# Kernel optimization log

Measured on AMD Instinct MI355X. Metric: run time of the kernel, lower is better.

Reference implementation:

```python
import jax, jax.numpy as jnp
import numpy as np

# Irreps: in1 = 128x0e + 64x1o + 32x2e, in2 = 16x0e (one-hot-style species attr),
# out = 128x0e + 64x1o + 32x2e.  (mul_in, mul_out, l) per CG path (l x 0e -> l).
PATHS = [(128, 128, 0), (64, 64, 1), (32, 32, 2)]
N_SPECIES = 16
N_NODES = 200_000
DIM_IN = sum(u * (2 * l + 1) for u, _, l in PATHS)   # 480
DIM_OUT = sum(w * (2 * l + 1) for _, w, l in PATHS)  # 480


def setup_inputs() -> dict:
    key = jax.random.key(0)
    k = jax.random.split(key, 5)
    return {
        "x": jax.random.normal(k[0], (N_NODES, DIM_IN), dtype=jnp.float32),
        "operand": jax.random.uniform(k[1], (N_NODES, N_SPECIES), dtype=jnp.float32),
        "w0": jax.random.normal(k[2], (128, N_SPECIES, 128), dtype=jnp.float32),
        "w1": jax.random.normal(k[3], (64, N_SPECIES, 64), dtype=jnp.float32),
        "w2": jax.random.normal(k[4], (32, N_SPECIES, 32), dtype=jnp.float32),
    }


def _path(xl, operand, W, alpha):
    # out[z,w,k] = alpha * sum_{u,v} xl[z,u,k] * operand[z,v] * W[u,v,w]
    # Scan over the small species axis v to avoid a huge [Z,u,w] intermediate.
    Z, u, d = xl.shape
    wm = W.shape[2]

    def step(acc, vin):
        Wv, ov = vin  # Wv: [u, w_out], ov: [Z]
        return acc + ov[:, None, None] * jnp.einsum('zuk,uw->zwk', xl, Wv), None

    init = jnp.zeros((Z, wm, d), dtype=xl.dtype)
    out, _ = jax.lax.scan(step, init, (jnp.moveaxis(W, 1, 0), operand.T))
    return alpha * out


def _fctp(x, operand, weights):
    # e3nn FullyConnectedTensorProduct with in2 = pure 0e scalars:
    # w3j(l, 0, l) = I / sqrt(2l+1); path_weight (component/element norm)
    # = sqrt((2l+1) / (mul_in * n_species))  ->  net alpha = 1/sqrt(mul_in*n_species).
    outs, off = [], 0
    for (u, wm, l), W in zip(PATHS, weights):
        d = 2 * l + 1
        xl = x[:, off:off + u * d].reshape(-1, u, d)  # [Z, mul_in, 2l+1]
        off += u * d
        alpha = jnp.float32(1.0 / float(np.sqrt(u * operand.shape[1])))
        out_l = _path(xl, operand, W, alpha)          # [Z, mul_out, 2l+1]
        outs.append(out_l.reshape(-1, wm * d))
    return jnp.concatenate(outs, axis=-1)             # [Z, 480]


def reference(x, operand, w0, w1, w2):
    return _fctp(x, operand, (w0, w1, w2))
```

## Files before the change

kernel.cpp:

```cpp
#include <hip/hip_runtime.h>
#include <stdint.h>


typedef __attribute__((ext_vector_type(8))) short bf16x8;
typedef __attribute__((ext_vector_type(4))) float f32x4;

__device__ __forceinline__ unsigned short f2bf(float f) {
    unsigned int u = __float_as_uint(f);
    u += 0x7fffu + ((u >> 16) & 1u);
    return (unsigned short)(u >> 16);
}
__device__ __forceinline__ unsigned int pack2(float a, float b) {
    return (unsigned int)f2bf(a) | ((unsigned int)f2bf(b) << 16);
}

__global__ void prep_wt(const float* __restrict__ w0, const float* __restrict__ w1,
                        const float* __restrict__ w2, unsigned short* __restrict__ wt) {
    int i = blockIdx.x * 256 + threadIdx.x;
    if (i < 262144) {
        int kk = i & 2047;
        int w  = i >> 11;
        wt[i] = f2bf(w0[kk * 128 + w]);
    } else if (i < 327680) {
        int r = i - 262144;
        int kk = r & 1023, w = r >> 10;
        wt[i] = f2bf(w1[kk * 64 + w]);
    } else if (i < 344064) {
        int r = i - 327680;
        int kk = r & 511, w = r >> 9;
        wt[i] = f2bf(w2[kk * 32 + w]);
    }
}

template<int D, int OFF, int K, int BN, int BM, int WAVES_M, int WAVES_N>
__global__ __launch_bounds__(256, 2)
void fctp_gemm(const float* __restrict__ x, const float* __restrict__ op,
               const unsigned short* __restrict__ wt, float* __restrict__ out,
               int Z, float alpha)
{
    constexpr int BK   = 32;
    constexpr int LDA  = BK + 8;
    constexpr int NSTEP = K / BK;
    constexpr int WTM  = BM / WAVES_M;
    constexpr int WTN  = BN / WAVES_N;
    constexpr int TM   = WTM / 16;
    constexpr int TN   = WTN / 16;

    __shared__ unsigned short Asm_[BM * LDA];
    __shared__ unsigned short Bsm_[BN * LDA];

    const int tid = threadIdx.x;
    const int M   = Z * D;
    const long m0 = (long)blockIdx.x * BM;

    int arow, usel;
    if constexpr (BM == 128) { arow = tid & 127; usel = tid >> 7; }
    else                     { arow = tid;       usel = 0;        }

    long mr = m0 + arow;
    if (mr >= M) mr = M - 1;
    const int zr = (int)(mr / D);
    const int kr = (int)(mr % D);

    float oreg[16];
    #pragma unroll
    for (int v = 0; v < 16; ++v) oreg[v] = op[(size_t)zr * 16 + v];

    const float* xp = x + (size_t)zr * 480 + OFF + kr + usel * D;

    f32x4 acc[TM][TN];
    #pragma unroll
    for (int i = 0; i < TM; ++i)
        #pragma unroll
        for (int j = 0; j < TN; ++j) acc[i][j] = f32x4{0.f, 0.f, 0.f, 0.f};

    const int lane = tid & 63;
    const int wv   = tid >> 6;
    const int wm0  = (wv / WAVES_N) * WTM;
    const int wn0  = (wv % WAVES_N) * WTN;
    const int q    = lane >> 4;
    const int l16  = lane & 15;

    for (int s = 0; s < NSTEP; ++s) {
        const int k0 = s * BK;
        __syncthreads();

        constexpr int BTOT = BN * 4;
        #pragma unroll
        for (int it = 0; it < (BTOT + 255) / 256; ++it) {
            int idx = it * 256 + tid;
            if ((BTOT % 256 == 0) || (idx < BTOT)) {
                int n = idx >> 2, qq = idx & 3;
                *(uint4*)(&Bsm_[n * LDA + qq * 8]) =
                    *(const uint4*)(wt + (size_t)n * K + k0 + qq * 8);
            }
        }

        if constexpr (BM == 128) {
            float xv = *xp; xp += 2 * D;
            unsigned int pk[8];
            #pragma unroll
            for (int vv = 0; vv < 8; ++vv)
                pk[vv] = pack2(xv * oreg[2 * vv], xv * oreg[2 * vv + 1]);
            uint4* dst = (uint4*)(&Asm_[arow * LDA + usel * 16]);
            dst[0] = uint4{pk[0], pk[1], pk[2], pk[3]};
            dst[1] = uint4{pk[4], pk[5], pk[6], pk[7]};
        } else {
            float xv0 = xp[0], xv1 = xp[D]; xp += 2 * D;
            unsigned int pk[16];
            #pragma unroll
            for (int vv = 0; vv < 8; ++vv) {
                pk[vv]     = pack2(xv0 * oreg[2 * vv], xv0 * oreg[2 * vv + 1]);
                pk[8 + vv] = pack2(xv1 * oreg[2 * vv], xv1 * oreg[2 * vv + 1]);
            }
            uint4* dst = (uint4*)(&Asm_[arow * LDA]);
            dst[0] = uint4{pk[0],  pk[1],  pk[2],  pk[3]};
            dst[1] = uint4{pk[4],  pk[5],  pk[6],  pk[7]};
            dst[2] = uint4{pk[8],  pk[9],  pk[10], pk[11]};
            dst[3] = uint4{pk[12], pk[13], pk[14], pk[15]};
        }
        __syncthreads();

        bf16x8 af[TM], bfr[TN];
        #pragma unroll
        for (int i = 0; i < TM; ++i)
            af[i] = *(const bf16x8*)(&Asm_[(wm0 + i * 16 + l16) * LDA + q * 8]);
        #pragma unroll
        for (int j = 0; j < TN; ++j)
            bfr[j] = *(const bf16x8*)(&Bsm_[(wn0 + j * 16 + l16) * LDA + q * 8]);
        #pragma unroll
        for (int i = 0; i < TM; ++i)
            #pragma unroll
            for (int j = 0; j < TN; ++j)
                acc[i][j] = __builtin_amdgcn_mfma_f32_16x16x32_bf16(
                    af[i], bfr[j], acc[i][j], 0, 0, 0);
    }

    #pragma unroll
    for (int i = 0; i < TM; ++i) {
        #pragma unroll
        for (int p = 0; p < 4; ++p) {
            long m = m0 + wm0 + i * 16 + q * 4 + p;
            if (m < M) {
                int z = (int)(m / D);
                int k = (int)(m % D);
                float* orow = out + (size_t)z * 480 + OFF + k;
                #pragma unroll
                for (int j = 0; j < TN; ++j) {
                    int col = wn0 + j * 16 + l16;
                    orow[col * D] = alpha * acc[i][j][p];
                }
            }
        }
    }
}

extern "C" void kernel_launch(void* const* d_in, const int* in_sizes, int n_in,
                              void* d_out, int out_size, void* d_ws, size_t ws_size,
                              hipStream_t stream) {
    (void)n_in; (void)out_size; (void)ws_size;
    const float* x  = (const float*)d_in[0];
    const float* op = (const float*)d_in[1];
    const float* w0 = (const float*)d_in[2];
    const float* w1 = (const float*)d_in[3];
    const float* w2 = (const float*)d_in[4];
    float* out = (float*)d_out;
    const int Z = in_sizes[0] / 480;

    unsigned short* wt = (unsigned short*)d_ws;
    prep_wt<<<1344, 256, 0, stream>>>(w0, w1, w2, wt);

    const unsigned short* wt0 = wt;
    const unsigned short* wt1 = wt + 262144;
    const unsigned short* wt2 = wt + 327680;

    {
        int M = Z, BM = 128;
        fctp_gemm<1, 0, 2048, 128, 128, 2, 2>
            <<<(M + BM - 1) / BM, 256, 0, stream>>>(x, op, wt0, out, Z, 0.02209708691f);
    }
    {
        int M = Z * 3, BM = 256;
        fctp_gemm<3, 128, 1024, 64, 256, 2, 2>
            <<<(M + BM - 1) / BM, 256, 0, stream>>>(x, op, wt1, out, Z, 0.03125f);
    }
    {
        int M = Z * 5, BM = 256;
        fctp_gemm<5, 320, 512, 32, 256, 4, 1>
            <<<(M + BM - 1) / BM, 256, 0, stream>>>(x, op, wt2, out, Z, 0.04419417382f);
    }
}
```

Baseline: 910.4 us.

## Double-buffer GEMM with async global-to-LDS weight loads, fp16 MFMA, swizzled LDS

Restructures the per-path GEMM main loop to double-buffer the A and B tiles in shared memory. B tiles are fetched with asynchronous global_load_lds DMA from a pre-swizzled weight layout, which removes the padded LDS rows and the register round trip. BK grows from 32 to 64, and the A operand (x times operand outer product) is built with packed fp16 multiplies instead of manual bf16 rounding, feeding f16 MFMA. The aim is to overlap the next tile's loads and A construction with the current MFMAs and to halve the number of barriers. In exchange it adds fp16 range and precision risk and uses more LDS per block.

```diff
diff --git a/kernel.cpp b/kernel.cpp
--- a/kernel.cpp
+++ b/kernel.cpp
@@ -2,34 +2,37 @@
 #include <stdint.h>
 
 
-typedef __attribute__((ext_vector_type(8))) short bf16x8;
+typedef __attribute__((ext_vector_type(8))) _Float16 f16x8;
+typedef __attribute__((ext_vector_type(2))) _Float16 f16x2;
 typedef __attribute__((ext_vector_type(4))) float f32x4;
-
-__device__ __forceinline__ unsigned short f2bf(float f) {
-    unsigned int u = __float_as_uint(f);
-    u += 0x7fffu + ((u >> 16) & 1u);
-    return (unsigned short)(u >> 16);
-}
-__device__ __forceinline__ unsigned int pack2(float a, float b) {
-    return (unsigned int)f2bf(a) | ((unsigned int)f2bf(b) << 16);
-}
 
 __global__ void prep_wt(const float* __restrict__ w0, const float* __restrict__ w1,
                         const float* __restrict__ w2, unsigned short* __restrict__ wt) {
     int i = blockIdx.x * 256 + threadIdx.x;
+    int n, kk, BN, base;
+    float v;
     if (i < 262144) {
-        int kk = i & 2047;
-        int w  = i >> 11;
-        wt[i] = f2bf(w0[kk * 128 + w]);
+        base = 0;      n = i >> 11; kk = i & 2047; BN = 128;
+        v = w0[kk * 128 + n];
     } else if (i < 327680) {
         int r = i - 262144;
-        int kk = r & 1023, w = r >> 10;
-        wt[i] = f2bf(w1[kk * 64 + w]);
-    } else if (i < 344064) {
+        base = 262144; n = r >> 10; kk = r & 1023; BN = 64;
+        v = w1[kk * 64 + n];
+    } else {
         int r = i - 327680;
-        int kk = r & 511, w = r >> 9;
-        wt[i] = f2bf(w2[kk * 32 + w]);
-    }
+        base = 327680; n = r >> 9;  kk = r & 511;  BN = 32;
+        v = w2[kk * 32 + n];
+    }
+    int t = kk >> 6, c = kk & 63;
+    union { _Float16 h; unsigned short s; } u;
+    u.h = (_Float16)v;
+    wt[base + (t * BN + n) * 64 + (c ^ ((n & 7) * 8))] = u.s;
+}
+
+__device__ __forceinline__ void gl_lds16(const void* g, void* l) {
+    __builtin_amdgcn_global_load_lds(
+        (const __attribute__((address_space(1))) unsigned int*)g,
+        (__attribute__((address_space(3))) unsigned int*)l, 16, 0, 0);
 }
 
 template<int D, int OFF, int K, int BN, int BM, int WAVES_M, int WAVES_N>
@@ -38,16 +41,17 @@
                const unsigned short* __restrict__ wt, float* __restrict__ out,
                int Z, float alpha)
 {
-    constexpr int BK   = 32;
-    constexpr int LDA  = BK + 8;
+    constexpr int BK    = 64;
     constexpr int NSTEP = K / BK;
-    constexpr int WTM  = BM / WAVES_M;
-    constexpr int WTN  = BN / WAVES_N;
-    constexpr int TM   = WTM / 16;
-    constexpr int TN   = WTN / 16;
-
-    __shared__ unsigned short Asm_[BM * LDA];
-    __shared__ unsigned short Bsm_[BN * LDA];
+    constexpr int WTM   = BM / WAVES_M;
+    constexpr int WTN   = BN / WAVES_N;
+    constexpr int TM    = WTM / 16;
+    constexpr int TN    = WTN / 16;
+    constexpr int CPW   = BN / 32;
+    constexpr int NXL   = (BM == 128) ? 2 : 4;
+
+    __shared__ unsigned short Asm_[2][BM * 64];
+    __shared__ unsigned short Bsm_[2][BN * 64];
 
     const int tid = threadIdx.x;
     const int M   = Z * D;
@@ -62,17 +66,16 @@
     const int zr = (int)(mr / D);
     const int kr = (int)(mr % D);
 
-    float oreg[16];
+    f16x2 oh[8];
     #pragma unroll
-    for (int v = 0; v < 16; ++v) oreg[v] = op[(size_t)zr * 16 + v];
-
-    const float* xp = x + (size_t)zr * 480 + OFF + kr + usel * D;
-
-    f32x4 acc[TM][TN];
-    #pragma unroll
-    for (int i = 0; i < TM; ++i)
-        #pragma unroll
-        for (int j = 0; j < TN; ++j) acc[i][j] = f32x4{0.f, 0.f, 0.f, 0.f};
+    for (int j = 0; j < 8; ++j) {
+        float a = op[(size_t)zr * 16 + 2 * j];
+        float b = op[(size_t)zr * 16 + 2 * j + 1];
+        oh[j] = f16x2{(_Float16)a, (_Float16)b};
+    }
+
+    const float* xbase = x + (size_t)zr * 480 + OFF + kr;
+    if constexpr (BM == 128) xbase += usel * 2 * D;
 
     const int lane = tid & 63;
     const int wv   = tid >> 6;
@@ -81,59 +84,86 @@
     const int q    = lane >> 4;
     const int l16  = lane & 15;
 
-    for (int s = 0; s < NSTEP; ++s) {
-        const int k0 = s * BK;
-        __syncthreads();
-
-        constexpr int BTOT = BN * 4;
-        #pragma unroll
-        for (int it = 0; it < (BTOT + 255) / 256; ++it) {
-            int idx = it * 256 + tid;
-            if ((BTOT % 256 == 0) || (idx < BTOT)) {
-                int n = idx >> 2, qq = idx & 3;
-                *(uint4*)(&Bsm_[n * LDA + qq * 8]) =
-                    *(const uint4*)(wt + (size_t)n * K + k0 + qq * 8);
-            }
-        }
-
-        if constexpr (BM == 128) {
-            float xv = *xp; xp += 2 * D;
+    f32x4 acc[TM][TN];
+    #pragma unroll
+    for (int i = 0; i < TM; ++i)
+        #pragma unroll
+        for (int j = 0; j < TN; ++j) acc[i][j] = f32x4{0.f, 0.f, 0.f, 0.f};
+
+    float xr[NXL];
+
+    auto xload = [&](int tt) {
+        #pragma unroll
+        for (int u = 0; u < NXL; ++u) xr[u] = xbase[(size_t)tt * 4 * D + u * D];
+    };
+
+    auto buildA = [&](int buf) {
+        unsigned short* rowp = &Asm_[buf][arow * 64];
+        const int swz = (arow & 7) * 8;
+        #pragma unroll
+        for (int u = 0; u < NXL; ++u) {
+            _Float16 xh = (_Float16)xr[u];
+            f16x2 xb2{xh, xh};
             unsigned int pk[8];
             #pragma unroll
-            for (int vv = 0; vv < 8; ++vv)
-                pk[vv] = pack2(xv * oreg[2 * vv], xv * oreg[2 * vv + 1]);
-            uint4* dst = (uint4*)(&Asm_[arow * LDA + usel * 16]);
-            dst[0] = uint4{pk[0], pk[1], pk[2], pk[3]};
-            dst[1] = uint4{pk[4], pk[5], pk[6], pk[7]};
-        } else {
-            float xv0 = xp[0], xv1 = xp[D]; xp += 2 * D;
-            unsigned int pk[16];
-            #pragma unroll
-            for (int vv = 0; vv < 8; ++vv) {
-                pk[vv]     = pack2(xv0 * oreg[2 * vv], xv0 * oreg[2 * vv + 1]);
-                pk[8 + vv] = pack2(xv1 * oreg[2 * vv], xv1 * oreg[2 * vv + 1]);
-            }
-            uint4* dst = (uint4*)(&Asm_[arow * LDA]);
-            dst[0] = uint4{pk[0],  pk[1],  pk[2],  pk[3]};
-            dst[1] = uint4{pk[4],  pk[5],  pk[6],  pk[7]};
-            dst[2] = uint4{pk[8],  pk[9],  pk[10], pk[11]};
-            dst[3] = uint4{pk[12], pk[13], pk[14], pk[15]};
-        }
-        __syncthreads();
-
-        bf16x8 af[TM], bfr[TN];
-        #pragma unroll
-        for (int i = 0; i < TM; ++i)
-            af[i] = *(const bf16x8*)(&Asm_[(wm0 + i * 16 + l16) * LDA + q * 8]);
-        #pragma unroll
-        for (int j = 0; j < TN; ++j)
-            bfr[j] = *(const bf16x8*)(&Bsm_[(wn0 + j * 16 + l16) * LDA + q * 8]);
-        #pragma unroll
-        for (int i = 0; i < TM; ++i)
-            #pragma unroll
-            for (int j = 0; j < TN; ++j)
-                acc[i][j] = __builtin_amdgcn_mfma_f32_16x16x32_bf16(
-                    af[i], bfr[j], acc[i][j], 0, 0, 0);
+            for (int j = 0; j < 8; ++j) {
+                f16x2 p = xb2 * oh[j];
+                pk[j] = __builtin_bit_cast(unsigned int, p);
+            }
+            const int cbase = (BM == 128 ? usel * 32 : 0) + u * 16;
+            *(uint4*)(rowp + ((cbase    ) ^ swz)) = uint4{pk[0], pk[1], pk[2], pk[3]};
+            *(uint4*)(rowp + ((cbase + 8) ^ swz)) = uint4{pk[4], pk[5], pk[6], pk[7]};
+        }
+    };
+
+    auto dmaB = [&](int buf, int tt) {
+        const unsigned short* src = wt + (size_t)tt * BN * 64;
+        unsigned short* dst = &Bsm_[buf][0];
+        #pragma unroll
+        for (int c = 0; c < CPW; ++c) {
+            int off = (wv * CPW + c) * 512 + lane * 8;
+            gl_lds16(src + off, dst + off);
+        }
+    };
+
+    auto compute = [&](int buf) {
+        #pragma unroll
+        for (int h = 0; h < 2; ++h) {
+            f16x8 af[TM], bfr[TN];
+            #pragma unroll
+            for (int i = 0; i < TM; ++i) {
+                int row = wm0 + i * 16 + l16;
+                af[i] = *(const f16x8*)(&Asm_[buf][row * 64 + ((h * 32 + q * 8) ^ ((row & 7) * 8))]);
+            }
+            #pragma unroll
+            for (int j = 0; j < TN; ++j) {
+                int n = wn0 + j * 16 + l16;
+                bfr[j] = *(const f16x8*)(&Bsm_[buf][n * 64 + ((h * 32 + q * 8) ^ ((n & 7) * 8))]);
+            }
+            #pragma unroll
+            for (int i = 0; i < TM; ++i)
+                #pragma unroll
+                for (int j = 0; j < TN; ++j)
+                    acc[i][j] = __builtin_amdgcn_mfma_f32_16x16x32_f16(
+                        af[i], bfr[j], acc[i][j], 0, 0, 0);
+        }
+    };
+
+    xload(0);
+    dmaB(0, 0);
+    buildA(0);
+    xload(1);
+    __syncthreads();
+
+    for (int t = 0; t < NSTEP; ++t) {
+        if (t + 1 < NSTEP) {
+            int nb = (t + 1) & 1;
+            dmaB(nb, t + 1);
+            buildA(nb);
+            xload(t + 2 < NSTEP ? t + 2 : NSTEP - 1);
+        }
+        compute(t & 1);
+        if (t + 1 < NSTEP) __syncthreads();
     }
 
     #pragma unroll
@@ -148,7 +178,7 @@
                 #pragma unroll
                 for (int j = 0; j < TN; ++j) {
                     int col = wn0 + j * 16 + l16;
-                    orow[col * D] = alpha * acc[i][j][p];
+                    orow[(size_t)col * D] = alpha * acc[i][j][p];
                 }
             }
         }
```

Measured after the change: 896.5 us. No clear change (-1.5%).
